# Optimization experiments

Hardware: AMD Instinct MI355X
Metric: run time of the kernel (lower is better)

The kernel has to match this reference:

```python
import jax, jax.numpy as jnp
import numpy as np

B = 131072   # batch
K = 3        # kernel size (= stride)
NP = 9       # num patches (9x9 image, 3x3 kernel, stride 3)
NU = 81      # num logic units/kernels
NOPS = 16    # real-valued binary logic ops


def setup_inputs() -> dict:
    key = jax.random.key(0)
    k1, k2, k3, k4 = jax.random.split(key, 4)
    x = jax.random.uniform(k1, (B, 1, 9, 9), dtype=jnp.float32)          # soft-binary image
    sel_a_logits = jax.random.normal(k2, (NU, K * K), dtype=jnp.float32)  # input-A selector per unit
    sel_b_logits = jax.random.normal(k3, (NU, K * K), dtype=jnp.float32)  # input-B selector per unit
    op_logits = jax.random.normal(k4, (NU, NOPS), dtype=jnp.float32)      # logic-op mixture per unit
    return {"x": x, "sel_a_logits": sel_a_logits, "sel_b_logits": sel_b_logits, "op_logits": op_logits}


def _soft_logic_mix(a, b, w):
    # a, b: [B, NU] soft-binary operands; w: [NU, 16] op mixture weights (broadcast over batch).
    # The 16 real-valued binary logic gates (Petersen et al. differentiable logic networks).
    ab = a * b
    return (w[:, 1] * ab
            + w[:, 2] * (a - ab)
            + w[:, 3] * a
            + w[:, 4] * (b - ab)
            + w[:, 5] * b
            + w[:, 6] * (a + b - 2.0 * ab)      # xor
            + w[:, 7] * (a + b - ab)            # or
            + w[:, 8] * (1.0 - (a + b - ab))    # nor
            + w[:, 9] * (1.0 - (a + b - 2.0 * ab))  # xnor
            + w[:, 10] * (1.0 - b)
            + w[:, 11] * (1.0 - b + ab)
            + w[:, 12] * (1.0 - a)
            + w[:, 13] * (1.0 - a + ab)
            + w[:, 14] * (1.0 - ab)             # nand
            + w[:, 15])                          # op 0 contributes 0


def reference(x, sel_a_logits, sel_b_logits, op_logits):
    b_sz = x.shape[0]
    img = x[:, 0]  # [B, 9, 9]
    # unfold(2,K,S).unfold(3,K,S) with S == K == 3 -> non-overlapping 3x3 patches, row-major patch order
    patches = img.reshape(b_sz, NP // K, K, NP // K, K)
    patches = patches.transpose(0, 1, 3, 2, 4).reshape(b_sz, NP, K * K)  # [B, 9, 9]
    # unit u uses patch u // kernels_per_pos (kernels_per_pos = 81 // 9 = 9)
    unit2patch = jnp.arange(NU) // (NU // NP)
    inp = patches[:, unit2patch]  # [B, 81, 9]
    a = jnp.einsum('bui,ui->bu', inp, jax.nn.softmax(sel_a_logits, axis=-1))  # [B, 81]
    b = jnp.einsum('bui,ui->bu', inp, jax.nn.softmax(sel_b_logits, axis=-1))  # [B, 81]
    w = jax.nn.softmax(op_logits, axis=-1)  # [81, 16]
    return _soft_logic_mix(a, b, w)  # [B, 81]
```

## Files before the change

kernel.cpp:

```cpp
#include <hip/hip_runtime.h>
#include <math.h>


#define NB      131072
#define NUNITS  81
#define BPB     64
#define THREADS 256
#define NBLK    (NB / BPB)
#define REC     24
#define CHUNKS  1296

__global__ __launch_bounds__(THREADS)
void logic_fused_kernel(const float* __restrict__ x,
                        const float* __restrict__ sa_logits,
                        const float* __restrict__ sb_logits,
                        const float* __restrict__ op_logits,
                        float* __restrict__ out)
{
    __shared__ float s_tile[BPB * 81];
    __shared__ float s_tab[NUNITS * REC];

    const int tid   = threadIdx.x;
    const int lane  = tid & 63;
    const int wavei = __builtin_amdgcn_readfirstlane(tid >> 6);
    const size_t b0 = (size_t)blockIdx.x * BPB;

    if (wavei < 3) {
        const float4* gsrc = (const float4*)(x + b0 * 81);
        float4* s4 = (float4*)s_tile;
        const int t3 = wavei * 64 + lane;
        #pragma unroll
        for (int k = 0; k < 7; ++k) {
            int j = t3 + k * 192;
            if (j < CHUNKS) s4[j] = gsrc[j];
        }
    } else {
        for (int u = lane; u < NUNITS; u += 64) {
            float v[9], m = -1e30f;
            #pragma unroll
            for (int i = 0; i < 9; ++i) { v[i] = sa_logits[u * 9 + i]; m = fmaxf(m, v[i]); }
            float s = 0.f;
            #pragma unroll
            for (int i = 0; i < 9; ++i) { v[i] = expf(v[i] - m); s += v[i]; }
            const float r = 1.f / s;
            #pragma unroll
            for (int i = 0; i < 9; ++i) s_tab[u * REC + i] = v[i] * r;
        }
        for (int u = lane; u < NUNITS; u += 64) {
            float v[9], m = -1e30f;
            #pragma unroll
            for (int i = 0; i < 9; ++i) { v[i] = sb_logits[u * 9 + i]; m = fmaxf(m, v[i]); }
            float s = 0.f;
            #pragma unroll
            for (int i = 0; i < 9; ++i) { v[i] = expf(v[i] - m); s += v[i]; }
            const float r = 1.f / s;
            #pragma unroll
            for (int i = 0; i < 9; ++i) s_tab[u * REC + 9 + i] = v[i] * r;
        }
        for (int u = lane; u < NUNITS; u += 64) {
            float v[16], m = -1e30f;
            #pragma unroll
            for (int i = 0; i < 16; ++i) { v[i] = op_logits[u * 16 + i]; m = fmaxf(m, v[i]); }
            float s = 0.f;
            #pragma unroll
            for (int i = 0; i < 16; ++i) { v[i] = expf(v[i] - m); s += v[i]; }
            const float r = 1.f / s;
            #pragma unroll
            for (int i = 0; i < 16; ++i) v[i] *= r;
            const float cab = v[1] - v[2] - v[4] - 2.f*v[6] - v[7] + v[8] + 2.f*v[9]
                            + v[11] + v[13] - v[14];
            const float ca  = v[2] + v[3] + v[6] + v[7] - v[8] - v[9] - v[12] - v[13];
            const float cb  = v[4] + v[5] + v[6] + v[7] - v[8] - v[9] - v[10] - v[11];
            const float c0  = v[8] + v[9] + v[10] + v[11] + v[12] + v[13] + v[14] + v[15];
            s_tab[u * REC + 18] = cab;
            s_tab[u * REC + 19] = ca;
            s_tab[u * REC + 20] = cb;
            s_tab[u * REC + 21] = c0;
        }
    }

    __syncthreads();

    if (wavei < 3) {
        float* my = s_tile + lane * 81 + wavei * 27;

        float in[27];
        #pragma unroll
        for (int j = 0; j < 27; ++j) in[j] = my[j];

        const float* __restrict__ wt = s_tab + wavei * 27 * REC;

        #pragma unroll
        for (int j = 0; j < 27; ++j) {
            const int q = j / 9;
            const float* __restrict__ wr = wt + j * REC;
            float a = 0.f, b = 0.f;
            #pragma unroll
            for (int i = 0; i < 9; ++i) {
                const float xi = in[q * 3 + (i / 3) * 9 + (i % 3)];
                a = fmaf(xi, wr[i],     a);
                b = fmaf(xi, wr[9 + i], b);
            }
            const float ab = a * b;
            my[j] = fmaf(wr[18], ab, fmaf(wr[19], a, fmaf(wr[20], b, wr[21])));
        }
    }

    __syncthreads();

    {
        const float4* s4 = (const float4*)s_tile;
        float4* gdst = (float4*)(out + b0 * 81);
        #pragma unroll
        for (int k = 0; k < 6; ++k) {
            int j = tid + k * THREADS;
            if (j < CHUNKS) gdst[j] = s4[j];
        }
    }
}

extern "C" void kernel_launch(void* const* d_in, const int* in_sizes, int n_in,
                              void* d_out, int out_size, void* d_ws, size_t ws_size,
                              hipStream_t stream)
{
    const float* x  = (const float*)d_in[0];
    const float* sa = (const float*)d_in[1];
    const float* sb = (const float*)d_in[2];
    const float* op = (const float*)d_in[3];
    float* outp = (float*)d_out;

    logic_fused_kernel<<<NBLK, THREADS, 0, stream>>>(x, sa, sb, op, outp);
}
```

Before: 30.65 us.

## Make kernel persistent and load input tiles directly into LDS

Launches a fixed grid of 1280 persistent blocks that loop over the 64-sample tiles, so the three softmax tables are built once per block instead of once per tile. Input tiles are fetched with global_load_lds 16-byte transfers straight into shared memory, skipping the trip through registers. Tiles do not divide evenly over the blocks, so some blocks process two tiles and others one. Each tile's load still waits for the previous tile's store, so loads and compute do not overlap.

Measured after the change: 28.39 us. -7.4%, faster.

```diff
diff --git a/kernel.cpp b/kernel.cpp
--- a/kernel.cpp
+++ b/kernel.cpp
@@ -6,16 +6,20 @@
 #define NUNITS  81
 #define BPB     64
 #define THREADS 256
-#define NBLK    (NB / BPB)
+#define NTILES  (NB / BPB)
+#define PBLK    1280
 #define REC     24
-#define CHUNKS  1296
+#define CHUNKS  (BPB * 81 / 4)
 
-__global__ __launch_bounds__(THREADS)
-void logic_fused_kernel(const float* __restrict__ x,
-                        const float* __restrict__ sa_logits,
-                        const float* __restrict__ sb_logits,
-                        const float* __restrict__ op_logits,
-                        float* __restrict__ out)
+typedef __attribute__((address_space(1))) const void GAS;
+typedef __attribute__((address_space(3))) void LAS;
+
+__global__ __launch_bounds__(THREADS, 5)
+void logic_fused_persistent(const float* __restrict__ x,
+                            const float* __restrict__ sa_logits,
+                            const float* __restrict__ sb_logits,
+                            const float* __restrict__ op_logits,
+                            float* __restrict__ out)
 {
     __shared__ float s_tile[BPB * 81];
     __shared__ float s_tab[NUNITS * REC];
@@ -23,16 +27,20 @@
     const int tid   = threadIdx.x;
     const int lane  = tid & 63;
     const int wavei = __builtin_amdgcn_readfirstlane(tid >> 6);
-    const size_t b0 = (size_t)blockIdx.x * BPB;
+
+    const int t0 = blockIdx.x;
 
     if (wavei < 3) {
-        const float4* gsrc = (const float4*)(x + b0 * 81);
-        float4* s4 = (float4*)s_tile;
+        const float4* gsrc = (const float4*)(x + (size_t)t0 * BPB * 81);
         const int t3 = wavei * 64 + lane;
         #pragma unroll
         for (int k = 0; k < 7; ++k) {
-            int j = t3 + k * 192;
-            if (j < CHUNKS) s4[j] = gsrc[j];
+            const int j = t3 + k * 192;
+            if (j < CHUNKS) {
+                float* lbase = s_tile + (size_t)(k * 192 + wavei * 64) * 4;
+                __builtin_amdgcn_global_load_lds((GAS*)(gsrc + j), (LAS*)lbase,
+                                                 16, 0, 0);
+            }
         }
     } else {
         for (int u = lane; u < NUNITS; u += 64) {
@@ -79,43 +87,60 @@
         }
     }
 
-    __syncthreads();
+    for (int t = t0; t < NTILES; t += PBLK) {
+        const size_t b0 = (size_t)t * BPB;
 
-    if (wavei < 3) {
-        float* my = s_tile + lane * 81 + wavei * 27;
+        if (t != t0) {
+            const float4* gsrc = (const float4*)(x + b0 * 81);
+            #pragma unroll
+            for (int k = 0; k < 6; ++k) {
+                const int j = tid + k * THREADS;
+                if (j < CHUNKS) {
+                    float* lbase = s_tile + (size_t)(k * THREADS + wavei * 64) * 4;
+                    __builtin_amdgcn_global_load_lds((GAS*)(gsrc + j), (LAS*)lbase,
+                                                     16, 0, 0);
+                }
+            }
+        }
+        __syncthreads();
 
-        float in[27];
-        #pragma unroll
-        for (int j = 0; j < 27; ++j) in[j] = my[j];
+        if (wavei < 3) {
+            float* my = s_tile + lane * 81 + wavei * 27;
 
-        const float* __restrict__ wt = s_tab + wavei * 27 * REC;
+            float in[27];
+            #pragma unroll
+            for (int j = 0; j < 27; ++j) in[j] = my[j];
 
-        #pragma unroll
-        for (int j = 0; j < 27; ++j) {
-            const int q = j / 9;
-            const float* __restrict__ wr = wt + j * REC;
-            float a = 0.f, b = 0.f;
+            const float* __restrict__ wt = s_tab + wavei * 27 * REC;
+
             #pragma unroll
-            for (int i = 0; i < 9; ++i) {
-                const float xi = in[q * 3 + (i / 3) * 9 + (i % 3)];
-                a = fmaf(xi, wr[i],     a);
-                b = fmaf(xi, wr[9 + i], b);
+            for (int j = 0; j < 27; ++j) {
+                const int q = j / 9;
+                const float* __restrict__ wr = wt + j * REC;
+                float a = 0.f, b = 0.f;
+                #pragma unroll
+                for (int i = 0; i < 9; ++i) {
+                    const float xi = in[q * 3 + (i / 3) * 9 + (i % 3)];
+                    a = fmaf(xi, wr[i],     a);
+                    b = fmaf(xi, wr[9 + i], b);
+                }
+                my[j] = fmaf(wr[18], a * b, fmaf(wr[19], a, fmaf(wr[20], b, wr[21])));
             }
-            const float ab = a * b;
-            my[j] = fmaf(wr[18], ab, fmaf(wr[19], a, fmaf(wr[20], b, wr[21])));
         }
-    }
 
-    __syncthreads();
+        __syncthreads();
 
-    {
-        const float4* s4 = (const float4*)s_tile;
-        float4* gdst = (float4*)(out + b0 * 81);
-        #pragma unroll
-        for (int k = 0; k < 6; ++k) {
-            int j = tid + k * THREADS;
-            if (j < CHUNKS) gdst[j] = s4[j];
+        {
+            const float4* s4 = (const float4*)s_tile;
+            float4* gdst = (float4*)(out + b0 * 81);
+            #pragma unroll
+            for (int k = 0; k < 6; ++k) {
+                const int j = tid + k * THREADS;
+                if (j < CHUNKS) gdst[j] = s4[j];
+            }
         }
+
+        __syncthreads();
     }
 }
 
@@ -129,5 +154,5 @@
     const float* op = (const float*)d_in[3];
     float* outp = (float*)d_out;
 
-    logic_fused_kernel<<<NBLK, THREADS, 0, stream>>>(x, sa, sb, op, outp);
+    logic_fused_persistent<<<PBLK, THREADS, 0, stream>>>(x, sa, sb, op, outp);
 }
```
